# Kernel optimization log

Hardware: AMD Instinct MI355X
Metric: run time of the kernel (lower is better)

Reference implementation:

```python
import jax, jax.numpy as jnp
import numpy as np

VOCAB = 512
D = 256          # hardcoded 256 in the inner_padding branch of the original module
S = 512          # seq_len (<= max_len of PositionalEmbedding)
B = 512          # batch
MAX_LEN = 512
SEP_ID = 13      # separator token triggering pad-aware indexing
PAD_ID = 1       # inner padding token


def _make_pe():
    # Sinusoidal table, identical to PositionalEmbedding.__init__
    pos = np.arange(MAX_LEN, dtype=np.float32)[:, None]
    div = np.exp(np.arange(0, D, 2, dtype=np.float32) * (-np.log(10000.0) / D))
    pe = np.zeros((MAX_LEN, D), dtype=np.float32)
    pe[:, 0::2] = np.sin(pos * div)
    pe[:, 1::2] = np.cos(pos * div)
    return jnp.asarray(pe)


def setup_inputs() -> dict:
    key = jax.random.key(0)
    k1, k2 = jax.random.split(key)
    sequence = jax.random.randint(k1, (S, B), 0, VOCAB)  # [seq, batch] int
    token_W = jax.random.normal(k2, (VOCAB, D), dtype=jnp.float32) * 0.02
    token_W = token_W.at[0].set(0.0)  # padding_idx=0 row is zero
    pe = _make_pe()
    return {"sequence": sequence, "token_W": token_W, "pe": pe}


def reference(sequence, token_W, pe):
    # Token embedding with padding_idx=0 (zero row, zero grad via mask).
    tok_emb = token_W[sequence] * (sequence != 0)[..., None].astype(token_W.dtype)  # [S,B,D]

    S_, B_ = sequence.shape

    # Vectorized version of the inner_padding host loop:
    # state machine per batch column over the sequence dim.
    def step(carry, xs):
        prev_sep, pad_num = carry              # [B] bool, [B] int32
        tok, j = xs                            # [B] token ids, scalar position
        is_sep = tok == SEP_ID
        skip = prev_sep & (tok == PAD_ID) & (~is_sep)  # inner pad after separator
        pos_emb = pe[j - pad_num]              # [B, D] gather with pad-adjusted index
        emb = jnp.where(skip[:, None], jnp.zeros((), pe.dtype), pos_emb)
        new_carry = (is_sep | skip, pad_num + skip.astype(pad_num.dtype))
        return new_carry, emb

    init = (jnp.zeros((B_,), dtype=bool), jnp.zeros((B_,), dtype=jnp.int32))
    _, pos_emb = jax.lax.scan(step, init, (sequence, jnp.arange(S_, dtype=jnp.int32)))

    # Dropout is identity in eval mode; step=None returns full output.
    return tok_emb + pos_emb  # [S, B, D]
```

## Files before the change

kernel.cpp:

```cpp
#include <hip/hip_runtime.h>

#define S_LEN 512
#define B_SZ  512
#define D_DIM 256
#define SEP_ID 13
#define PAD_ID 1

#define NTHR   256
#define ROWS_PER_WAVE 32
#define ROWS_PER_BLOCK 128
#define NROWS  (S_LEN * B_SZ)
#define NBLK   (NROWS / ROWS_PER_BLOCK)

typedef float f32x4 __attribute__((ext_vector_type(4)));

__global__ void emb_scan_wave(const int* __restrict__ seq,
                              int* __restrict__ idx) {
    const int lane = threadIdx.x & 63;
    const int b = blockIdx.x * (blockDim.x >> 6) + (threadIdx.x >> 6);
    if (b >= B_SZ) return;

    const int s0 = lane * (S_LEN / 64);
    int toks[8];
#pragma unroll
    for (int k = 0; k < 8; ++k) toks[k] = seq[(s0 + k) * B_SZ + b];

    unsigned A = 0u, Bf = 1u;
#pragma unroll
    for (int k = 0; k < 8; ++k) {
        unsigned a  = (toks[k] == SEP_ID) ? 1u : 0u;
        unsigned bb = (toks[k] == PAD_ID) ? 1u : 0u;
        A  = a | (A & bb);
        Bf = Bf & bb;
    }

    unsigned incA = A, incB = Bf;
    for (int d = 1; d < 64; d <<= 1) {
        unsigned Al = __shfl_up(incA, d, 64);
        unsigned Bl = __shfl_up(incB, d, 64);
        if (lane >= d) {
            incA = incA | (Al & incB);
            incB = Bl & incB;
        }
    }
    unsigned pin = __shfl_up(incA, 1, 64);
    if (lane == 0) pin = 0u;

    unsigned p = pin, skipbits = 0u;
    int cnt = 0;
#pragma unroll
    for (int k = 0; k < 8; ++k) {
        unsigned a  = (toks[k] == SEP_ID) ? 1u : 0u;
        unsigned bb = (toks[k] == PAD_ID) ? 1u : 0u;
        unsigned skip = p & bb;
        skipbits |= skip << k;
        cnt += (int)skip;
        p = a | skip;
    }

    int pref = cnt;
    for (int d = 1; d < 64; d <<= 1) {
        int v = __shfl_up(pref, d, 64);
        if (lane >= d) pref += v;
    }
    pref -= cnt;

    int pad = pref;
#pragma unroll
    for (int k = 0; k < 8; ++k) {
        int s = s0 + k;
        unsigned skip = (skipbits >> k) & 1u;
        idx[s * B_SZ + b] = skip ? -1 : (s - pad);
        pad += (int)skip;
    }
}

__global__ void __launch_bounds__(NTHR)
emb_fused_kernel(const int* __restrict__ seq,
                 const float* __restrict__ tw,
                 const float* __restrict__ pe,
                 const int* __restrict__ idx,
                 float* __restrict__ out) {
    const unsigned lane  = threadIdx.x & 63u;
    const unsigned wid_s = (unsigned)__builtin_amdgcn_readfirstlane(threadIdx.x >> 6);
    const unsigned row0  = blockIdx.x * ROWS_PER_BLOCK + wid_s * ROWS_PER_WAVE;
    const unsigned doff  = lane * 4u;

    const int* __restrict__ tokp  = seq + row0;
    const int* __restrict__ pidxp = idx + row0;
    float* orow = out + (size_t)row0 * D_DIM + doff;

#pragma unroll 8
    for (int it = 0; it < ROWS_PER_WAVE; ++it) {
        const int tok  = tokp[it];
        const int pidx = pidxp[it];

        const f32x4 tv = *(const f32x4*)(tw + (size_t)tok * D_DIM + doff);
        const int   pc = (pidx < 0) ? 0 : pidx;
        const f32x4 pv = *(const f32x4*)(pe + (size_t)pc * D_DIM + doff);
        const float pm = (pidx < 0) ? 0.0f : 1.0f;

        f32x4 o = tv + pv * pm;
        *(f32x4*)(orow + (size_t)it * D_DIM) = o;
    }
}

extern "C" void kernel_launch(void* const* d_in, const int* in_sizes, int n_in,
                              void* d_out, int out_size, void* d_ws, size_t ws_size,
                              hipStream_t stream) {
    const int*   seq = (const int*)d_in[0];
    const float* tw  = (const float*)d_in[1];
    const float* pe  = (const float*)d_in[2];
    float* out = (float*)d_out;
    int*   idx = (int*)d_ws;

    emb_scan_wave<<<dim3(B_SZ / 4), dim3(256), 0, stream>>>(seq, idx);

    emb_fused_kernel<<<dim3(NBLK), dim3(NTHR), 0, stream>>>(seq, tw, pe, idx, out);
}
```

Before: 53.40 us.

## Pack token and position index into one word; fast path for unskipped waves

The scan kernel now writes the token id and the position index plus one packed into a single 32-bit word, so the main kernel reads one index array instead of two. Each wave checks whether all 32 of its rows share the unshifted position of their sequence row. If they do, it loads that positional row once and skips the per-row pe gather and masking. This removes index traffic and redundant pe loads, at the cost of an extra 32-element pre-check per wave and the assumption that token ids fit in 16 bits.

```diff
diff --git a/kernel.cpp b/kernel.cpp
--- a/kernel.cpp
+++ b/kernel.cpp
@@ -15,7 +15,7 @@
 typedef float f32x4 __attribute__((ext_vector_type(4)));
 
 __global__ void emb_scan_wave(const int* __restrict__ seq,
-                              int* __restrict__ idx) {
+                              unsigned* __restrict__ pack) {
     const int lane = threadIdx.x & 63;
     const int b = blockIdx.x * (blockDim.x >> 6) + (threadIdx.x >> 6);
     if (b >= B_SZ) return;
@@ -70,38 +70,55 @@
     for (int k = 0; k < 8; ++k) {
         int s = s0 + k;
         unsigned skip = (skipbits >> k) & 1u;
-        idx[s * B_SZ + b] = skip ? -1 : (s - pad);
+        unsigned p1 = skip ? 0u : (unsigned)(s - pad + 1);
+        pack[s * B_SZ + b] = (unsigned)toks[k] | (p1 << 16);
         pad += (int)skip;
     }
 }
 
 __global__ void __launch_bounds__(NTHR)
-emb_fused_kernel(const int* __restrict__ seq,
+emb_fused_kernel(const unsigned* __restrict__ pack,
                  const float* __restrict__ tw,
                  const float* __restrict__ pe,
-                 const int* __restrict__ idx,
                  float* __restrict__ out) {
     const unsigned lane  = threadIdx.x & 63u;
     const unsigned wid_s = (unsigned)__builtin_amdgcn_readfirstlane(threadIdx.x >> 6);
     const unsigned row0  = blockIdx.x * ROWS_PER_BLOCK + wid_s * ROWS_PER_WAVE;
+    const unsigned s_row = row0 >> 9;
     const unsigned doff  = lane * 4u;
 
-    const int* __restrict__ tokp  = seq + row0;
-    const int* __restrict__ pidxp = idx + row0;
+    const unsigned* __restrict__ packp = pack + row0;
     float* orow = out + (size_t)row0 * D_DIM + doff;
 
+    const f32x4 pv_s = *(const f32x4*)(pe + (size_t)s_row * D_DIM + doff);
+
+    const unsigned want = (s_row + 1u) << 16;
+    bool clean = true;
+#pragma unroll
+    for (int it = 0; it < ROWS_PER_WAVE; ++it)
+        clean = clean && ((packp[it] & 0xFFFF0000u) == want);
+
+    if (clean) {
 #pragma unroll 8
-    for (int it = 0; it < ROWS_PER_WAVE; ++it) {
-        const int tok  = tokp[it];
-        const int pidx = pidxp[it];
+        for (int it = 0; it < ROWS_PER_WAVE; ++it) {
+            const unsigned tok = packp[it] & 0xFFFFu;
+            const f32x4 tv = *(const f32x4*)(tw + (size_t)tok * D_DIM + doff);
+            *(f32x4*)(orow + (size_t)it * D_DIM) = tv + pv_s;
+        }
+    } else {
+#pragma unroll 8
+        for (int it = 0; it < ROWS_PER_WAVE; ++it) {
+            const unsigned m   = packp[it];
+            const unsigned tok = m & 0xFFFFu;
+            const int      p1  = (int)(m >> 16);
 
-        const f32x4 tv = *(const f32x4*)(tw + (size_t)tok * D_DIM + doff);
-        const int   pc = (pidx < 0) ? 0 : pidx;
-        const f32x4 pv = *(const f32x4*)(pe + (size_t)pc * D_DIM + doff);
-        const float pm = (pidx < 0) ? 0.0f : 1.0f;
+            const f32x4 tv = *(const f32x4*)(tw + (size_t)tok * D_DIM + doff);
+            const int   pc = (p1 <= 0) ? 0 : (p1 - 1);
+            const f32x4 pv = *(const f32x4*)(pe + (size_t)pc * D_DIM + doff);
+            const float pm = (p1 == 0) ? 0.0f : 1.0f;
 
-        f32x4 o = tv + pv * pm;
-        *(f32x4*)(orow + (size_t)it * D_DIM) = o;
+            *(f32x4*)(orow + (size_t)it * D_DIM) = tv + pv * pm;
+        }
     }
 }
 
@@ -112,9 +129,9 @@
     const float* tw  = (const float*)d_in[1];
     const float* pe  = (const float*)d_in[2];
     float* out = (float*)d_out;
-    int*   idx = (int*)d_ws;
+    unsigned* pack = (unsigned*)d_ws;
 
-    emb_scan_wave<<<dim3(B_SZ / 4), dim3(256), 0, stream>>>(seq, idx);
+    emb_scan_wave<<<dim3(B_SZ / 4), dim3(256), 0, stream>>>(seq, pack);
 
-    emb_fused_kernel<<<dim3(NBLK), dim3(NTHR), 0, stream>>>(seq, tw, pe, idx, out);
+    emb_fused_kernel<<<dim3(NBLK), dim3(NTHR), 0, stream>>>(pack, tw, pe, out);
 }
```

Result: slower. 57.32 us (+7.3%).

## Restructure pad-index scan to lane-per-column with two-level block scan

Applied to the files above, without the earlier changes.

The scan kernel no longer gives each batch column its own wave with a shuffle-based parallel prefix over sequence chunks. Now each lane owns a column, so reads and writes of seq/idx are coalesced across lanes. The four waves each cover 128 sequence positions, and their summaries (carry state and pad counts for both possible incoming states) are combined through shared memory. The intent is to remove the uncoalesced strided access and the shuffle overhead. In exchange the launch shrinks to 8 blocks with long serial per-thread loops, which gives low occupancy on a large GPU.

```diff
diff --git a/kernel.cpp b/kernel.cpp
--- a/kernel.cpp
+++ b/kernel.cpp
@@ -14,64 +14,57 @@
 
 typedef float f32x4 __attribute__((ext_vector_type(4)));
 
-__global__ void emb_scan_wave(const int* __restrict__ seq,
-                              int* __restrict__ idx) {
+__global__ void __launch_bounds__(256)
+emb_scan_2level(const int* __restrict__ seq, int* __restrict__ idx) {
     const int lane = threadIdx.x & 63;
-    const int b = blockIdx.x * (blockDim.x >> 6) + (threadIdx.x >> 6);
-    if (b >= B_SZ) return;
+    const int w    = threadIdx.x >> 6;
+    const int col  = blockIdx.x * 64 + lane;
+    const int sbase = w * 128;
 
-    const int s0 = lane * (S_LEN / 64);
-    int toks[8];
+    __shared__ unsigned summ[4][64];
+
+    unsigned sepb[4], padb[4];
+    unsigned p0 = 0u, p1 = 1u, c0 = 0u, c1 = 0u;
 #pragma unroll
-    for (int k = 0; k < 8; ++k) toks[k] = seq[(s0 + k) * B_SZ + b];
+    for (int q = 0; q < 4; ++q) {
+        unsigned sb = 0u, pb = 0u;
+#pragma unroll
+        for (int j = 0; j < 32; ++j) {
+            const int t = seq[(sbase + q * 32 + j) * B_SZ + col];
+            const unsigned is_sep = (t == SEP_ID) ? 1u : 0u;
+            const unsigned is_pad = (t == PAD_ID) ? 1u : 0u;
+            sb |= is_sep << j;
+            pb |= is_pad << j;
+            const unsigned k0 = p0 & is_pad; c0 += k0; p0 = is_sep | k0;
+            const unsigned k1 = p1 & is_pad; c1 += k1; p1 = is_sep | k1;
+        }
+        sepb[q] = sb;
+        padb[q] = pb;
+    }
+    summ[w][lane] = p0 | (p1 << 1) | (c0 << 8) | (c1 << 20);
+    __syncthreads();
 
-    unsigned A = 0u, Bf = 1u;
-#pragma unroll
-    for (int k = 0; k < 8; ++k) {
-        unsigned a  = (toks[k] == SEP_ID) ? 1u : 0u;
-        unsigned bb = (toks[k] == PAD_ID) ? 1u : 0u;
-        A  = a | (A & bb);
-        Bf = Bf & bb;
+    unsigned p = 0u, padn = 0u;
+    for (int ww = 0; ww < w; ++ww) {
+        const unsigned sm = summ[ww][lane];
+        padn += p ? ((sm >> 20) & 0xFFFu) : ((sm >> 8) & 0xFFFu);
+        p = p ? ((sm >> 1) & 1u) : (sm & 1u);
     }
 
-    unsigned incA = A, incB = Bf;
-    for (int d = 1; d < 64; d <<= 1) {
-        unsigned Al = __shfl_up(incA, d, 64);
-        unsigned Bl = __shfl_up(incB, d, 64);
-        if (lane >= d) {
-            incA = incA | (Al & incB);
-            incB = Bl & incB;
+#pragma unroll
+    for (int q = 0; q < 4; ++q) {
+        const unsigned sb = sepb[q];
+        const unsigned pb = padb[q];
+#pragma unroll
+        for (int j = 0; j < 32; ++j) {
+            const unsigned is_sep = (sb >> j) & 1u;
+            const unsigned is_pad = (pb >> j) & 1u;
+            const unsigned sk = p & is_pad;
+            const int s = sbase + q * 32 + j;
+            idx[s * B_SZ + col] = sk ? -1 : (int)(s - padn);
+            padn += sk;
+            p = is_sep | sk;
         }
-    }
-    unsigned pin = __shfl_up(incA, 1, 64);
-    if (lane == 0) pin = 0u;
-
-    unsigned p = pin, skipbits = 0u;
-    int cnt = 0;
-#pragma unroll
-    for (int k = 0; k < 8; ++k) {
-        unsigned a  = (toks[k] == SEP_ID) ? 1u : 0u;
-        unsigned bb = (toks[k] == PAD_ID) ? 1u : 0u;
-        unsigned skip = p & bb;
-        skipbits |= skip << k;
-        cnt += (int)skip;
-        p = a | skip;
-    }
-
-    int pref = cnt;
-    for (int d = 1; d < 64; d <<= 1) {
-        int v = __shfl_up(pref, d, 64);
-        if (lane >= d) pref += v;
-    }
-    pref -= cnt;
-
-    int pad = pref;
-#pragma unroll
-    for (int k = 0; k < 8; ++k) {
-        int s = s0 + k;
-        unsigned skip = (skipbits >> k) & 1u;
-        idx[s * B_SZ + b] = skip ? -1 : (s - pad);
-        pad += (int)skip;
     }
 }
 
@@ -114,7 +107,7 @@
     float* out = (float*)d_out;
     int*   idx = (int*)d_ws;
 
-    emb_scan_wave<<<dim3(B_SZ / 4), dim3(256), 0, stream>>>(seq, idx);
+    emb_scan_2level<<<dim3(B_SZ / 64), dim3(256), 0, stream>>>(seq, idx);
 
     emb_fused_kernel<<<dim3(NBLK), dim3(NTHR), 0, stream>>>(seq, tw, pe, idx, out);
 }
```

Result: slower. 95.21 us (+78.3%).

## Fuse pad-aware scan and embedding gather into a single per-batch kernel

Applied to the files above, without the earlier changes.

The separate scan kernel and gather kernel are merged into one launch with one block per batch column. Wave 0 computes the pad-adjusted positions and packs token and position into shared memory, then all four waves read that metadata and write output rows. This removes a kernel launch and the global index buffer round trip. In exchange, three waves idle during the serial scan, only 512 blocks are launched, and output stores now jump by B*D floats between rows instead of being contiguous across rows.

```diff
diff --git a/kernel.cpp b/kernel.cpp
--- a/kernel.cpp
+++ b/kernel.cpp
@@ -6,102 +6,93 @@
 #define SEP_ID 13
 #define PAD_ID 1
 
-#define NTHR   256
-#define ROWS_PER_WAVE 32
-#define ROWS_PER_BLOCK 128
-#define NROWS  (S_LEN * B_SZ)
-#define NBLK   (NROWS / ROWS_PER_BLOCK)
-
 typedef float f32x4 __attribute__((ext_vector_type(4)));
 
-__global__ void emb_scan_wave(const int* __restrict__ seq,
-                              int* __restrict__ idx) {
+__global__ void __launch_bounds__(256)
+emb_onekernel(const int* __restrict__ seq,
+              const float* __restrict__ tw,
+              const float* __restrict__ pe,
+              float* __restrict__ out) {
+    const int b    = blockIdx.x;
     const int lane = threadIdx.x & 63;
-    const int b = blockIdx.x * (blockDim.x >> 6) + (threadIdx.x >> 6);
-    if (b >= B_SZ) return;
+    const int w    = threadIdx.x >> 6;
 
-    const int s0 = lane * (S_LEN / 64);
-    int toks[8];
+    __shared__ unsigned meta[S_LEN];
+
+    if (w == 0) {
+        const int s0 = lane * (S_LEN / 64);
+        int toks[8];
 #pragma unroll
-    for (int k = 0; k < 8; ++k) toks[k] = seq[(s0 + k) * B_SZ + b];
+        for (int k = 0; k < 8; ++k) toks[k] = seq[(s0 + k) * B_SZ + b];
 
-    unsigned A = 0u, Bf = 1u;
+        unsigned A = 0u, Bf = 1u;
 #pragma unroll
-    for (int k = 0; k < 8; ++k) {
-        unsigned a  = (toks[k] == SEP_ID) ? 1u : 0u;
-        unsigned bb = (toks[k] == PAD_ID) ? 1u : 0u;
-        A  = a | (A & bb);
-        Bf = Bf & bb;
-    }
+        for (int k = 0; k < 8; ++k) {
+            unsigned a  = (toks[k] == SEP_ID) ? 1u : 0u;
+            unsigned bb = (toks[k] == PAD_ID) ? 1u : 0u;
+            A  = a | (A & bb);
+            Bf = Bf & bb;
+        }
 
-    unsigned incA = A, incB = Bf;
-    for (int d = 1; d < 64; d <<= 1) {
-        unsigned Al = __shfl_up(incA, d, 64);
-        unsigned Bl = __shfl_up(incB, d, 64);
-        if (lane >= d) {
-            incA = incA | (Al & incB);
-            incB = Bl & incB;
+        unsigned incA = A, incB = Bf;
+        for (int d = 1; d < 64; d <<= 1) {
+            unsigned Al = __shfl_up(incA, d, 64);
+            unsigned Bl = __shfl_up(incB, d, 64);
+            if (lane >= d) {
+                incA = incA | (Al & incB);
+                incB = Bl & incB;
+            }
+        }
+        unsigned pin = __shfl_up(incA, 1, 64);
+        if (lane == 0) pin = 0u;
+
+        unsigned p = pin, skipbits = 0u;
+        int cnt = 0;
+#pragma unroll
+        for (int k = 0; k < 8; ++k) {
+            unsigned a  = (toks[k] == SEP_ID) ? 1u : 0u;
+            unsigned bb = (toks[k] == PAD_ID) ? 1u : 0u;
+            unsigned skip = p & bb;
+            skipbits |= skip << k;
+            cnt += (int)skip;
+            p = a | skip;
+        }
+
+        int pref = cnt;
+        for (int d = 1; d < 64; d <<= 1) {
+            int v = __shfl_up(pref, d, 64);
+            if (lane >= d) pref += v;
+        }
+        pref -= cnt;
+
+        int pad = pref;
+#pragma unroll
+        for (int k = 0; k < 8; ++k) {
+            int s = s0 + k;
+            unsigned skip = (skipbits >> k) & 1u;
+            unsigned p1 = skip ? 0u : (unsigned)(s - pad + 1);
+            meta[s] = (unsigned)toks[k] | (p1 << 16);
+            pad += (int)skip;
         }
     }
-    unsigned pin = __shfl_up(incA, 1, 64);
-    if (lane == 0) pin = 0u;
+    __syncthreads();
 
-    unsigned p = pin, skipbits = 0u;
-    int cnt = 0;
-#pragma unroll
-    for (int k = 0; k < 8; ++k) {
-        unsigned a  = (toks[k] == SEP_ID) ? 1u : 0u;
-        unsigned bb = (toks[k] == PAD_ID) ? 1u : 0u;
-        unsigned skip = p & bb;
-        skipbits |= skip << k;
-        cnt += (int)skip;
-        p = a | skip;
-    }
-
-    int pref = cnt;
-    for (int d = 1; d < 64; d <<= 1) {
-        int v = __shfl_up(pref, d, 64);
-        if (lane >= d) pref += v;
-    }
-    pref -= cnt;
-
-    int pad = pref;
-#pragma unroll
-    for (int k = 0; k < 8; ++k) {
-        int s = s0 + k;
-        unsigned skip = (skipbits >> k) & 1u;
-        idx[s * B_SZ + b] = skip ? -1 : (s - pad);
-        pad += (int)skip;
-    }
-}
-
-__global__ void __launch_bounds__(NTHR)
-emb_fused_kernel(const int* __restrict__ seq,
-                 const float* __restrict__ tw,
-                 const float* __restrict__ pe,
-                 const int* __restrict__ idx,
-                 float* __restrict__ out) {
-    const unsigned lane  = threadIdx.x & 63u;
-    const unsigned wid_s = (unsigned)__builtin_amdgcn_readfirstlane(threadIdx.x >> 6);
-    const unsigned row0  = blockIdx.x * ROWS_PER_BLOCK + wid_s * ROWS_PER_WAVE;
-    const unsigned doff  = lane * 4u;
-
-    const int* __restrict__ tokp  = seq + row0;
-    const int* __restrict__ pidxp = idx + row0;
-    float* orow = out + (size_t)row0 * D_DIM + doff;
+    const unsigned doff = (unsigned)lane * 4u;
+    float* ob = out + (size_t)b * D_DIM + doff;
 
 #pragma unroll 8
-    for (int it = 0; it < ROWS_PER_WAVE; ++it) {
-        const int tok  = tokp[it];
-        const int pidx = pidxp[it];
+    for (int i = 0; i < S_LEN / 4; ++i) {
+        const int s = w * (S_LEN / 4) + i;
+        const unsigned m   = meta[s];
+        const unsigned tok = m & 0xFFFFu;
+        const int      p1  = (int)(m >> 16);
 
         const f32x4 tv = *(const f32x4*)(tw + (size_t)tok * D_DIM + doff);
-        const int   pc = (pidx < 0) ? 0 : pidx;
+        const int   pc = (p1 > 0) ? (p1 - 1) : 0;
         const f32x4 pv = *(const f32x4*)(pe + (size_t)pc * D_DIM + doff);
-        const float pm = (pidx < 0) ? 0.0f : 1.0f;
+        const float pm = (p1 == 0) ? 0.0f : 1.0f;
 
-        f32x4 o = tv + pv * pm;
-        *(f32x4*)(orow + (size_t)it * D_DIM) = o;
+        *(f32x4*)(ob + (size_t)s * B_SZ * D_DIM) = tv + pv * pm;
     }
 }
 
@@ -112,9 +103,6 @@
     const float* tw  = (const float*)d_in[1];
     const float* pe  = (const float*)d_in[2];
     float* out = (float*)d_out;
-    int*   idx = (int*)d_ws;
 
-    emb_scan_wave<<<dim3(B_SZ / 4), dim3(256), 0, stream>>>(seq, idx);
-
-    emb_fused_kernel<<<dim3(NBLK), dim3(NTHR), 0, stream>>>(seq, tw, pe, idx, out);
+    emb_onekernel<<<dim3(B_SZ), dim3(256), 0, stream>>>(seq, tw, pe, out);
 }
```

Result: slower. 61.24 us (+14.7%).
